# Kernel optimization log

Measured on AMD Instinct MI355X. Metric: run time of the kernel, lower is better.

The kernel has to match this reference:

```python
import jax, jax.numpy as jnp
import numpy as np
import math

H = 12
D_MODEL = 768
D_K = D_MODEL // H


def setup_inputs() -> dict:
    key = jax.random.key(0)
    ks = jax.random.split(key, 12)
    B, L = 128, 512
    s = 1.0 / math.sqrt(D_MODEL)
    return {
        "Q": jax.random.normal(ks[0], (B, L, D_MODEL), jnp.float32),
        "K": jax.random.normal(ks[1], (B, L, D_MODEL), jnp.float32),
        "V": jax.random.normal(ks[2], (B, L, D_MODEL), jnp.float32),
        "mask": jax.random.uniform(ks[3], (B, B), jnp.float32),
        "Wq": jax.random.normal(ks[4], (D_MODEL, D_MODEL), jnp.float32) * s,
        "bq": jnp.zeros((D_MODEL,), jnp.float32),
        "Wk": jax.random.normal(ks[5], (D_MODEL, D_MODEL), jnp.float32) * s,
        "bk": jnp.zeros((D_MODEL,), jnp.float32),
        "Wv": jax.random.normal(ks[6], (D_MODEL, D_MODEL), jnp.float32) * s,
        "bv": jnp.zeros((D_MODEL,), jnp.float32),
        "Wo": jax.random.normal(ks[7], (D_MODEL, D_MODEL), jnp.float32) * s,
        "bo": jnp.zeros((D_MODEL,), jnp.float32),
    }


def reference(Q, K, V, mask, Wq, bq, Wk, bk, Wv, bv, Wo, bo):
    nb_q = Q.shape[0]   # nbatches_q = Q.size(0) in the torch code
    nb_kv = K.shape[0]
    # Linear projections then the module's exact reshape/transpose pattern.
    q = (Q @ Wq + bq).reshape(-1, nb_q, H, D_K).swapaxes(1, 2)   # (L, h, B, d_k)
    k = (K @ Wk + bk).reshape(-1, nb_kv, H, D_K).swapaxes(1, 2)  # (L, h, B, d_k)
    v = (V @ Wv + bv).reshape(-1, nb_kv, H, D_K).swapaxes(1, 2)  # (L, h, B, d_k)
    # AttentionAgger: model_dim = d_k -> scale by sqrt(d_k)
    attn = jnp.einsum('lhbd,lhed->lhbe', q, k) / math.sqrt(D_K)  # (L, h, B, B)
    # dual softmax with additive mask bias (mask scaled by its leading dim)
    m = jax.nn.softmax(mask / mask.shape[0], axis=-1)            # (B, B), broadcasts
    attn = jax.nn.softmax(attn, axis=-1) + m
    attn = jax.nn.softmax(attn, axis=-1)
    x = jnp.einsum('lhbe,lhed->lhbd', attn, v)                   # (L, h, B, d_k)
    x = x.swapaxes(1, 2).reshape(-1, nb_q, H * D_K)              # (L, B, d_model)
    return x @ Wo + bo
```

## Files before the change

### kernel.cpp

```cpp
#include <hip/hip_runtime.h>


typedef __attribute__((ext_vector_type(8))) __bf16 bf16x8;
typedef __attribute__((ext_vector_type(4))) __bf16 bf16x4;
typedef __attribute__((ext_vector_type(4))) float f32x4;

#define DM 768
#define LOG2E 1.44269504f

__device__ __forceinline__ unsigned short f2bf(float x) {
  unsigned u = __float_as_uint(x);
  u += 0x7FFFu + ((u >> 16) & 1u);
  return (unsigned short)(u >> 16);
}

__device__ __forceinline__ void gl_lds16(const void* g, void* l) {
  __builtin_amdgcn_global_load_lds(
      (const __attribute__((address_space(1))) unsigned int*)g,
      (__attribute__((address_space(3))) unsigned int*)l, 16, 0, 0);
}

__global__ __launch_bounds__(256) void prep_w(const float* __restrict__ w0,
                                              const float* __restrict__ w1,
                                              const float* __restrict__ w2,
                                              const float* __restrict__ w3,
                                              unsigned short* __restrict__ wt) {
  __shared__ float t[32][33];
  const int op = blockIdx.z;
  const float* w = (op == 0) ? w0 : (op == 1) ? w1 : (op == 2) ? w2 : w3;
  unsigned short* o = wt + (size_t)op * DM * DM;
  const int n0 = blockIdx.x * 32, k0 = blockIdx.y * 32;
  const int tx = threadIdx.x & 31, ty = threadIdx.x >> 5;
#pragma unroll
  for (int r = 0; r < 4; ++r)
    t[r * 8 + ty][tx] = w[(size_t)(k0 + r * 8 + ty) * DM + n0 + tx];
  __syncthreads();
#pragma unroll
  for (int r = 0; r < 4; ++r)
    o[(size_t)(n0 + r * 8 + ty) * DM + k0 + tx] = f2bf(t[tx][r * 8 + ty]);
}

__global__ void prep_m(const float* __restrict__ mask, float* __restrict__ mm) {
  int row = blockIdx.x;
  int t = threadIdx.x;
  float a = mask[row * 128 + t] * (1.0f / 128.0f);
  float b = mask[row * 128 + t + 64] * (1.0f / 128.0f);
  float mx = fmaxf(a, b);
  for (int s = 1; s < 64; s <<= 1) mx = fmaxf(mx, __shfl_xor(mx, s));
  float ea = __expf(a - mx), eb = __expf(b - mx);
  float sum = ea + eb;
  for (int s = 1; s < 64; s <<= 1) sum += __shfl_xor(sum, s);
  float inv = LOG2E / sum;
  mm[row * 128 + t] = ea * inv;
  mm[row * 128 + t + 64] = eb * inv;
}

__global__ __launch_bounds__(256) void convb(const float* __restrict__ in,
                                             unsigned short* __restrict__ out, int n8) {
  int i = blockIdx.x * 256 + threadIdx.x;
  const int stride = gridDim.x * 256;
  for (; i < n8; i += stride) {
    const float4 a = ((const float4*)in)[(size_t)i * 2];
    const float4 b = ((const float4*)in)[(size_t)i * 2 + 1];
    ushort4 lo = {f2bf(a.x), f2bf(a.y), f2bf(a.z), f2bf(a.w)};
    ushort4 hi = {f2bf(b.x), f2bf(b.y), f2bf(b.z), f2bf(b.w)};
    ((ushort4*)out)[(size_t)i * 2] = lo;
    ((ushort4*)out)[(size_t)i * 2 + 1] = hi;
  }
}

__device__ __forceinline__ void stage_tile(const unsigned short* __restrict__ src,
                                           int row0, int kcol, char* slotbase, int tid) {
  const int wid = tid >> 6, lane = tid & 63;
#pragma unroll
  for (int s = 0; s < 2; ++s) {
    const int row = s * 128 + wid * 16 + (lane >> 2);
    const int slot = lane & 3;
    gl_lds16(src + (size_t)(row0 + row) * DM + kcol + ((slot ^ ((row >> 1) & 3)) * 8),
             slotbase + s * 8192 + wid * 1024);
  }
}

template <bool OUT_BF16>
__global__ __launch_bounds__(512, 2) void gemm8(const unsigned short* __restrict__ A,
                                                const unsigned short* __restrict__ Bt,
                                                const float* __restrict__ bias,
                                                void* __restrict__ Outp) {
  __shared__ char smem[131072];
  const int tid = threadIdx.x, lane = tid & 63, wid = tid >> 6;
  const int cl = lane & 15, g = lane >> 4;
  const int wm = wid >> 2, wn = wid & 3;
  const int bid = blockIdx.x;
  const int xcd = bid & 7, bi = bid >> 3;
  const int m0 = (xcd * 32 + bi / 3) * 256;
  const int n0 = (bi % 3) * 256;

  f32x4 acc[8][4] = {};

  auto aslot = [&](int t) { return (char*)smem + (t & 3) * 16384; };
  auto bslot = [&](int t) { return (char*)smem + 65536 + (t & 3) * 16384; };

  auto lda = [&](bf16x8* af, int t, int half) {
#pragma unroll
    for (int mi = 0; mi < 4; ++mi) {
      const int r = wm * 128 + (half * 4 + mi) * 16 + cl;
      af[mi] = *(const bf16x8*)(aslot(t) + r * 64 + ((g ^ ((r >> 1) & 3)) * 16));
    }
  };
  auto ldb = [&](bf16x8* bf, int t) {
#pragma unroll
    for (int ni = 0; ni < 4; ++ni) {
      const int r = wn * 64 + ni * 16 + cl;
      bf[ni] = *(const bf16x8*)(bslot(t) + r * 64 + ((g ^ ((r >> 1) & 3)) * 16));
    }
  };
  auto mfma16 = [&](bf16x8* af, bf16x8* bf, int half) {
    __builtin_amdgcn_s_setprio(1);
#pragma unroll
    for (int mi = 0; mi < 4; ++mi)
#pragma unroll
      for (int ni = 0; ni < 4; ++ni)
        acc[half * 4 + mi][ni] = __builtin_amdgcn_mfma_f32_16x16x32_bf16(
            af[mi], bf[ni], acc[half * 4 + mi][ni], 0, 0, 0);
    __builtin_amdgcn_s_setprio(0);
  };

  auto gstep = [&](int t, bool stg, int vm, bf16x8* af0, bf16x8* bfc,
                   bf16x8* af0n, bf16x8* bfn, bool last) {
    bf16x8 af1[4];
    if (stg) stage_tile(A, m0, (t + 3) * 32, aslot(t + 3), tid);
    if (vm == 6)      asm volatile("s_waitcnt vmcnt(6)" ::: "memory");
    else if (vm == 4) asm volatile("s_waitcnt vmcnt(4)" ::: "memory");
    else              asm volatile("s_waitcnt vmcnt(0)" ::: "memory");
    __builtin_amdgcn_s_barrier();
    lda(af1, t, 1);
    mfma16(af0, bfc, 0);
    if (stg) stage_tile(Bt, n0, (t + 3) * 32, bslot(t + 3), tid);
    if (!last) {
      lda(af0n, t + 1, 0);
      ldb(bfn, t + 1);
    }
    mfma16(af1, bfc, 1);
    __builtin_amdgcn_s_barrier();
  };

  stage_tile(A, m0, 0, aslot(0), tid);   stage_tile(Bt, n0, 0, bslot(0), tid);
  stage_tile(A, m0, 32, aslot(1), tid);  stage_tile(Bt, n0, 32, bslot(1), tid);
  stage_tile(A, m0, 64, aslot(2), tid);  stage_tile(Bt, n0, 64, bslot(2), tid);
  asm volatile("s_waitcnt vmcnt(8)" ::: "memory");
  __builtin_amdgcn_s_barrier();

  bf16x8 afA[4], bfA[4], afB[4], bfB[4];
  lda(afA, 0, 0);
  ldb(bfA, 0);

#pragma unroll 1
  for (int t = 0; t < 20; t += 2) {
    gstep(t, true, 6, afA, bfA, afB, bfB, false);
    gstep(t + 1, true, 6, afB, bfB, afA, bfA, false);
  }
  gstep(20, true, 6, afA, bfA, afB, bfB, false);
  gstep(21, false, 4, afB, bfB, afA, bfA, false);
  gstep(22, false, 0, afA, bfA, afB, bfB, false);
  gstep(23, false, 0, afB, bfB, afA, bfA, true);

  float bb[4];
#pragma unroll
  for (int ni = 0; ni < 4; ++ni) bb[ni] = bias[n0 + wn * 64 + ni * 16 + cl];
#pragma unroll
  for (int mi = 0; mi < 8; ++mi) {
    const int row = m0 + wm * 128 + mi * 16 + g * 4;
#pragma unroll
    for (int ni = 0; ni < 4; ++ni) {
      const int col = n0 + wn * 64 + ni * 16 + cl;
#pragma unroll
      for (int e = 0; e < 4; ++e) {
        float v = acc[mi][ni][e] + bb[ni];
        if constexpr (OUT_BF16)
          ((unsigned short*)Outp)[(size_t)(row + e) * DM + col] = f2bf(v);
        else
          ((float*)Outp)[(size_t)(row + e) * DM + col] = v;
      }
    }
  }
}

__global__ __launch_bounds__(512) void attn_k(const unsigned short* __restrict__ qp,
                                              const unsigned short* __restrict__ kp,
                                              const unsigned short* __restrict__ vp,
                                              const float* __restrict__ mm,
                                              unsigned short* __restrict__ xout) {
  __shared__ char smem[32768];
  unsigned short* vt = (unsigned short*)(smem + 16384);

  const int tid = threadIdx.x, lane = tid & 63, wid = tid >> 6;
  const int cl = lane & 15, g = lane >> 4;
  const int h = blockIdx.x, l = blockIdx.y;
  const size_t base = (size_t)l * 128 * DM + h * 64;
  const int q = wid * 16 + cl;

#pragma unroll
  for (int p = 0; p < 2; ++p) {
    const int chunk = p * 8 + wid;
    const int row = chunk * 8 + (lane >> 3);
    const int gi = (lane & 7) ^ (row & 7);
    gl_lds16(kp + base + (size_t)row * DM + gi * 8, smem + chunk * 1024);
  }
  if (tid < 256) {
    const int dc = (tid & 7) * 8;
    const int kq = tid >> 3;
    int4 r0 = *(const int4*)&vp[base + (size_t)(kq * 4 + 0) * DM + dc];
    int4 r1 = *(const int4*)&vp[base + (size_t)(kq * 4 + 1) * DM + dc];
    int4 r2 = *(const int4*)&vp[base + (size_t)(kq * 4 + 2) * DM + dc];
    int4 r3 = *(const int4*)&vp[base + (size_t)(kq * 4 + 3) * DM + dc];
    const unsigned short* u0 = (const unsigned short*)&r0;
    const unsigned short* u1 = (const unsigned short*)&r1;
    const unsigned short* u2 = (const unsigned short*)&r2;
    const unsigned short* u3 = (const unsigned short*)&r3;
    const int pg = (kq >> 1) ^ ((tid & 1) << 2);
    const int ofs = (kq & 1) * 4;
#pragma unroll
    for (int j = 0; j < 8; ++j) {
      ushort4 w = {u0[j], u1[j], u2[j], u3[j]};
      *(ushort4*)&vt[(dc + j) * 128 + pg * 8 + ofs] = w;
    }
  }
  bf16x8 qf[2];
#pragma unroll
  for (int ksr = 0; ksr < 2; ++ksr)
    qf[ksr] = *(const bf16x8*)&qp[base + (size_t)q * DM + ksr * 32 + g * 8];
  __syncthreads();

  f32x4 sacc[8] = {};
  __builtin_amdgcn_s_setprio(1);
#pragma unroll
  for (int ksr = 0; ksr < 2; ++ksr) {
#pragma unroll
    for (int kf = 0; kf < 8; ++kf) {
      const int row = kf * 16 + cl;
      const int gi = (ksr * 4 + g) ^ (row & 7);
      bf16x8 kfr = *(const bf16x8*)(smem + row * 128 + gi * 16);
      sacc[kf] = __builtin_amdgcn_mfma_f32_16x16x32_bf16(kfr, qf[ksr], sacc[kf], 0, 0, 0);
    }
  }
  __builtin_amdgcn_s_setprio(0);
  __syncthreads();

  bf16x4 pk[8];
  {
    float4 mrow[8];
#pragma unroll
    for (int kf = 0; kf < 8; ++kf)
      mrow[kf] = *(const float4*)&mm[q * 128 + kf * 16 + g * 4];
    float sm = 0.f;
#pragma unroll
    for (int kf = 0; kf < 8; ++kf)
#pragma unroll
      for (int e = 0; e < 4; ++e) {
        float p = exp2f(sacc[kf][e] * (0.125f * LOG2E));
        sacc[kf][e] = p;
        sm += p;
      }
    sm += __shfl_xor(sm, 16); sm += __shfl_xor(sm, 32);
    const float inv2e = LOG2E / sm;
    float s2 = 0.f;
#pragma unroll
    for (int kf = 0; kf < 8; ++kf)
#pragma unroll
      for (int e = 0; e < 4; ++e) {
        float p = exp2f(fmaf(sacc[kf][e], inv2e, ((const float*)&mrow[kf])[e]));
        sacc[kf][e] = p;
        s2 += p;
      }
    s2 += __shfl_xor(s2, 16); s2 += __shfl_xor(s2, 32);
    const float inv2 = 1.0f / s2;
#pragma unroll
    for (int kf = 0; kf < 8; ++kf)
      pk[kf] = {(__bf16)(sacc[kf][0] * inv2), (__bf16)(sacc[kf][1] * inv2),
                (__bf16)(sacc[kf][2] * inv2), (__bf16)(sacc[kf][3] * inv2)};
  }

  f32x4 xacc[4] = {};
#pragma unroll
  for (int half = 0; half < 2; ++half) {
#pragma unroll
    for (int kf = 0; kf < 4; ++kf) {
      const int gi = (kf * 4 + g) ^ ((q & 3) << 2);
      *(bf16x4*)(smem + q * 128 + gi * 8) = pk[half * 4 + kf];
    }
    asm volatile("s_waitcnt lgkmcnt(0)" ::: "memory");
    __builtin_amdgcn_sched_barrier(0);
    __builtin_amdgcn_s_setprio(1);
#pragma unroll
    for (int k2 = 0; k2 < 2; ++k2) {
      const int ks2 = half * 2 + k2;
      const int gi = (k2 * 8 + g * 2) ^ ((q & 3) << 2);
      bf16x8 pa = *(const bf16x8*)(smem + q * 128 + gi * 8);
#pragma unroll
      for (int fc = 0; fc < 4; ++fc) {
        const int d = fc * 16 + cl;
        const int pg = (ks2 * 4 + g) ^ (((d >> 3) & 1) << 2);
        bf16x8 bv = *(const bf16x8*)&vt[d * 128 + pg * 8];
        xacc[fc] = __builtin_amdgcn_mfma_f32_16x16x32_bf16(pa, bv, xacc[fc], 0, 0, 0);
      }
    }
    __builtin_amdgcn_s_setprio(0);
    if (half == 0) {
      asm volatile("s_waitcnt lgkmcnt(0)" ::: "memory");
      __builtin_amdgcn_sched_barrier(0);
    }
  }

#pragma unroll
  for (int fc = 0; fc < 4; ++fc)
#pragma unroll
    for (int e = 0; e < 4; ++e) {
      const int qr = wid * 16 + g * 4 + e;
      __bf16 b = (__bf16)xacc[fc][e];
      unsigned short u;
      __builtin_memcpy(&u, &b, 2);
      xout[base + (size_t)qr * DM + fc * 16 + cl] = u;
    }
}

extern "C" void kernel_launch(void* const* d_in, const int* in_sizes, int n_in,
                              void* d_out, int out_size, void* d_ws, size_t ws_size,
                              hipStream_t stream) {
  (void)in_sizes; (void)n_in; (void)out_size; (void)ws_size;
  const float* Q = (const float*)d_in[0];
  const float* K = (const float*)d_in[1];
  const float* V = (const float*)d_in[2];
  const float* mask = (const float*)d_in[3];
  const float* Wq = (const float*)d_in[4];
  const float* bq = (const float*)d_in[5];
  const float* Wk = (const float*)d_in[6];
  const float* bk = (const float*)d_in[7];
  const float* Wv = (const float*)d_in[8];
  const float* bv = (const float*)d_in[9];
  const float* Wo = (const float*)d_in[10];
  const float* bo = (const float*)d_in[11];

  const size_t NP = (size_t)65536 * DM;

  unsigned short* qp = (unsigned short*)d_out;
  unsigned short* kp = qp + NP;
  unsigned short* S1 = (unsigned short*)d_ws;
  unsigned short* S2 = S1 + NP;
  unsigned short* wt = S2 + NP;
  float* mm = (float*)(wt + (size_t)4 * DM * DM);

  prep_w<<<dim3(24, 24, 4), 256, 0, stream>>>(Wq, Wk, Wv, Wo, wt);
  prep_m<<<dim3(128), 64, 0, stream>>>(mask, mm);

  const int n8 = (int)(NP / 8);
  dim3 g8(768);

  convb<<<dim3(2048), 256, 0, stream>>>(Q, S1, n8);
  gemm8<true><<<g8, 512, 0, stream>>>(S1, wt + 0 * (size_t)DM * DM, bq, qp);
  convb<<<dim3(2048), 256, 0, stream>>>(K, S1, n8);
  gemm8<true><<<g8, 512, 0, stream>>>(S1, wt + 1 * (size_t)DM * DM, bk, kp);
  convb<<<dim3(2048), 256, 0, stream>>>(V, S2, n8);
  gemm8<true><<<g8, 512, 0, stream>>>(S2, wt + 2 * (size_t)DM * DM, bv, S1);

  attn_k<<<dim3(12, 512), 512, 0, stream>>>(qp, kp, S1, mm, S1);

  gemm8<false><<<g8, 512, 0, stream>>>(S1, wt + 3 * (size_t)DM * DM, bo, (float*)d_out);
}
```

Baseline: 662.4 us.

## Batch Q/K conversions and projections into paired launches; reswizzle V-transpose LDS layout

Q and K bf16 conversion and their projection GEMMs now run as single launches with a grid y-dimension selecting the operand, and the V path uses the freed buffers. This doubles the grid per launch, which is meant to remove launch gaps and tail underutilisation between back-to-back kernels. Separately, the transposed V tile in the attention kernel gets a finer 4-element swizzle over 8 groups, meant to reduce LDS bank conflicts on the transpose writes and MFMA operand reads. The new swizzle must stay consistent between writer and reader.

New measurement: 669.4 us. Within noise of the previous version (+1.0%).

```diff
diff --git a/kernel.cpp b/kernel.cpp
--- a/kernel.cpp
+++ b/kernel.cpp
@@ -55,8 +55,8 @@
   mm[row * 128 + t + 64] = eb * inv;
 }
 
-__global__ __launch_bounds__(256) void convb(const float* __restrict__ in,
-                                             unsigned short* __restrict__ out, int n8) {
+__device__ __forceinline__ void convb_body(const float* __restrict__ in,
+                                           unsigned short* __restrict__ out, int n8) {
   int i = blockIdx.x * 256 + threadIdx.x;
   const int stride = gridDim.x * 256;
   for (; i < n8; i += stride) {
@@ -69,6 +69,19 @@
   }
 }
 
+__global__ __launch_bounds__(256) void convb(const float* __restrict__ in,
+                                             unsigned short* __restrict__ out, int n8) {
+  convb_body(in, out, n8);
+}
+
+__global__ __launch_bounds__(256) void convb2(const float* __restrict__ in0,
+                                              const float* __restrict__ in1,
+                                              unsigned short* __restrict__ out0,
+                                              unsigned short* __restrict__ out1, int n8) {
+  const int op = blockIdx.y;
+  convb_body(op ? in1 : in0, op ? out1 : out0, n8);
+}
+
 __device__ __forceinline__ void stage_tile(const unsigned short* __restrict__ src,
                                            int row0, int kcol, char* slotbase, int tid) {
   const int wid = tid >> 6, lane = tid & 63;
@@ -82,11 +95,10 @@
 }
 
 template <bool OUT_BF16>
-__global__ __launch_bounds__(512, 2) void gemm8(const unsigned short* __restrict__ A,
-                                                const unsigned short* __restrict__ Bt,
-                                                const float* __restrict__ bias,
-                                                void* __restrict__ Outp) {
-  __shared__ char smem[131072];
+__device__ __forceinline__ void gemm8_body(const unsigned short* __restrict__ A,
+                                           const unsigned short* __restrict__ Bt,
+                                           const float* __restrict__ bias,
+                                           void* __restrict__ Outp, char* smem) {
   const int tid = threadIdx.x, lane = tid & 63, wid = tid >> 6;
   const int cl = lane & 15, g = lane >> 4;
   const int wm = wid >> 2, wn = wid & 3;
@@ -97,8 +109,8 @@
 
   f32x4 acc[8][4] = {};
 
-  auto aslot = [&](int t) { return (char*)smem + (t & 3) * 16384; };
-  auto bslot = [&](int t) { return (char*)smem + 65536 + (t & 3) * 16384; };
+  auto aslot = [&](int t) { return smem + (t & 3) * 16384; };
+  auto bslot = [&](int t) { return smem + 65536 + (t & 3) * 16384; };
 
   auto lda = [&](bf16x8* af, int t, int half) {
 #pragma unroll
@@ -185,6 +197,29 @@
   }
 }
 
+template <bool OUT_BF16>
+__global__ __launch_bounds__(512, 2) void gemm8(const unsigned short* __restrict__ A,
+                                                const unsigned short* __restrict__ Bt,
+                                                const float* __restrict__ bias,
+                                                void* __restrict__ Outp) {
+  __shared__ char smem[131072];
+  gemm8_body<OUT_BF16>(A, Bt, bias, Outp, smem);
+}
+
+__global__ __launch_bounds__(512, 2) void gemm8x2(const unsigned short* __restrict__ A0,
+                                                  const unsigned short* __restrict__ Bt0,
+                                                  const float* __restrict__ b0,
+                                                  unsigned short* __restrict__ O0,
+                                                  const unsigned short* __restrict__ A1,
+                                                  const unsigned short* __restrict__ Bt1,
+                                                  const float* __restrict__ b1,
+                                                  unsigned short* __restrict__ O1) {
+  __shared__ char smem[131072];
+  const int op = blockIdx.y;
+  gemm8_body<true>(op ? A1 : A0, op ? Bt1 : Bt0, op ? b1 : b0,
+                   op ? (void*)O1 : (void*)O0, smem);
+}
+
 __global__ __launch_bounds__(512) void attn_k(const unsigned short* __restrict__ qp,
                                               const unsigned short* __restrict__ kp,
                                               const unsigned short* __restrict__ vp,
@@ -209,6 +244,7 @@
   if (tid < 256) {
     const int dc = (tid & 7) * 8;
     const int kq = tid >> 3;
+    const int pg = (kq ^ ((tid & 7) << 2));
     int4 r0 = *(const int4*)&vp[base + (size_t)(kq * 4 + 0) * DM + dc];
     int4 r1 = *(const int4*)&vp[base + (size_t)(kq * 4 + 1) * DM + dc];
     int4 r2 = *(const int4*)&vp[base + (size_t)(kq * 4 + 2) * DM + dc];
@@ -217,12 +253,10 @@
     const unsigned short* u1 = (const unsigned short*)&r1;
     const unsigned short* u2 = (const unsigned short*)&r2;
     const unsigned short* u3 = (const unsigned short*)&r3;
-    const int pg = (kq >> 1) ^ ((tid & 1) << 2);
-    const int ofs = (kq & 1) * 4;
 #pragma unroll
     for (int j = 0; j < 8; ++j) {
       ushort4 w = {u0[j], u1[j], u2[j], u3[j]};
-      *(ushort4*)&vt[(dc + j) * 128 + pg * 8 + ofs] = w;
+      *(ushort4*)&vt[(dc + j) * 128 + pg * 4] = w;
     }
   }
   bf16x8 qf[2];
@@ -299,8 +333,8 @@
 #pragma unroll
       for (int fc = 0; fc < 4; ++fc) {
         const int d = fc * 16 + cl;
-        const int pg = (ks2 * 4 + g) ^ (((d >> 3) & 1) << 2);
-        bf16x8 bv = *(const bf16x8*)&vt[d * 128 + pg * 8];
+        const int pg = (ks2 * 8 + 2 * g) ^ (((d >> 3) & 7) << 2);
+        bf16x8 bv = *(const bf16x8*)&vt[d * 128 + pg * 4];
         xacc[fc] = __builtin_amdgcn_mfma_f32_16x16x32_bf16(pa, bv, xacc[fc], 0, 0, 0);
       }
     }
@@ -353,16 +387,16 @@
   prep_m<<<dim3(128), 64, 0, stream>>>(mask, mm);
 
   const int n8 = (int)(NP / 8);
-  dim3 g8(768);
-
-  convb<<<dim3(2048), 256, 0, stream>>>(Q, S1, n8);
-  gemm8<true><<<g8, 512, 0, stream>>>(S1, wt + 0 * (size_t)DM * DM, bq, qp);
-  convb<<<dim3(2048), 256, 0, stream>>>(K, S1, n8);
-  gemm8<true><<<g8, 512, 0, stream>>>(S1, wt + 1 * (size_t)DM * DM, bk, kp);
-  convb<<<dim3(2048), 256, 0, stream>>>(V, S2, n8);
-  gemm8<true><<<g8, 512, 0, stream>>>(S2, wt + 2 * (size_t)DM * DM, bv, S1);
-
-  attn_k<<<dim3(12, 512), 512, 0, stream>>>(qp, kp, S1, mm, S1);
-
-  gemm8<false><<<g8, 512, 0, stream>>>(S1, wt + 3 * (size_t)DM * DM, bo, (float*)d_out);
-}
+
+  convb2<<<dim3(2048, 2), 256, 0, stream>>>(Q, K, S1, S2, n8);
+  gemm8x2<<<dim3(768, 2), 512, 0, stream>>>(S1, wt + 0 * (size_t)DM * DM, bq, qp,
+                                            S2, wt + 1 * (size_t)DM * DM, bk, kp);
+
+  convb<<<dim3(2048), 256, 0, stream>>>(V, S1, n8);
+  gemm8<true><<<dim3(768), 512, 0, stream>>>(S1, wt + 2 * (size_t)DM * DM, bv, S2);
+
+  attn_k<<<dim3(12, 512), 512, 0, stream>>>(qp, kp, S2, mm, S2);
+
+  gemm8<false><<<dim3(768), 512, 0, stream>>>(S2, wt + 3 * (size_t)DM * DM, bo,
+                                              (float*)d_out);
+}
```
